# Optimization experiments

Hardware: AMD Instinct MI355X
Metric: run time of the kernel (lower is better)

## Reference

```python
import jax, jax.numpy as jnp
import numpy as np

N_NODES = 100000
N_EDGES = 1600000
D_IN, D_HID, D_OUT = 128, 128, 64


def spmm(row, col, val, h, n):
    # y[i] = sum_{e: row[e]==i} val[e] * h[col[e]]  (A_hat @ h with A in COO form)
    return jax.ops.segment_sum(val[:, None] * h[col], row, num_segments=n)


def setup_inputs() -> dict:
    key = jax.random.key(0)
    ks = jax.random.split(key, 7)
    x = jax.random.normal(ks[0], (1, N_NODES, D_IN), dtype=jnp.float32)
    edge_row = jax.random.randint(ks[1], (N_EDGES,), 0, N_NODES, dtype=jnp.int32)
    edge_col = jax.random.randint(ks[2], (N_EDGES,), 0, N_NODES, dtype=jnp.int32)
    edge_val = jax.random.uniform(ks[3], (N_EDGES,), dtype=jnp.float32)
    W0 = jax.random.normal(ks[4], (D_HID, D_IN), dtype=jnp.float32) * 0.05
    W1 = jax.random.normal(ks[5], (D_HID, D_HID), dtype=jnp.float32) * 0.05
    W2 = jax.random.normal(ks[6], (D_OUT, D_HID), dtype=jnp.float32) * 0.05
    return {"x": x, "edge_row": edge_row, "edge_col": edge_col,
            "edge_val": edge_val, "W0": W0, "W1": W1, "W2": W2}


def reference(x, edge_row, edge_col, edge_val, W0, W1, W2):
    B, N, D = x.shape
    n = B * N
    h = x.reshape(n, D)
    # input conv: Linear (no bias) -> SpMM -> ReLU
    h = jax.nn.relu(spmm(edge_row, edge_col, edge_val, h @ W0.T, n))
    # hidden conv with residual: ReLU(A (h W1^T)) + h
    h = jax.nn.relu(spmm(edge_row, edge_col, edge_val, h @ W1.T, n)) + h
    # dropout is identity in eval mode
    out = spmm(edge_row, edge_col, edge_val, h @ W2.T, n)
    return out
```

## Files before the change

kernel.cpp:

```cpp
#include <hip/hip_runtime.h>


typedef unsigned int u32;
typedef unsigned short u16;
typedef __attribute__((ext_vector_type(8))) short bf16x8;
typedef __attribute__((ext_vector_type(4))) float f32x4;

constexpr int NN = 100000;
constexpr int NE = 1600000;
constexpr int PAD = 100352;
constexpr int NBUCK = 196;
constexpr int BCAP = 10240;
constexpr int EPB = 2048;

__device__ __forceinline__ u16 f2bf(float f) {
    u32 x = __float_as_uint(f);
    x += 0x7fffu + ((x >> 16) & 1u);
    return (u16)(x >> 16);
}

template<int DO, bool FP32IN>
__global__ __launch_bounds__(256)
void gemm_mfma(const void* __restrict__ Hin, const u16* __restrict__ Wf,
               u16* __restrict__ Cb, int n)
{
    constexpr int RS   = 136;
    constexpr int PADW = DO + 8;
    __shared__ u16 smem[64 * 136];
    u16* sA = smem;
    u16* sC = smem;

    const int tid  = threadIdx.x;
    const int w    = tid >> 6;
    const int lane = tid & 63;
    const int m    = lane & 15;
    const int q    = lane >> 4;
    const int rowBase = blockIdx.x * 64;

    if (FP32IN) {
        const float* H = (const float*)Hin;
        #pragma unroll
        for (int i = 0; i < 8; ++i) {
            const int g = (i * 256 + tid) * 4;
            const int r = g >> 7, c = g & 127;
            float4 v = make_float4(0.f, 0.f, 0.f, 0.f);
            if (rowBase + r < n) v = *(const float4*)(H + (size_t)(rowBase + r) * 128 + c);
            u16* d = &sA[r * RS + c];
            d[0] = f2bf(v.x); d[1] = f2bf(v.y); d[2] = f2bf(v.z); d[3] = f2bf(v.w);
        }
    } else {
        const u16* H = (const u16*)Hin;
        #pragma unroll
        for (int i = 0; i < 4; ++i) {
            const int g = (i * 256 + tid) * 8;
            const int r = g >> 7, c = g & 127;
            uint4 v = make_uint4(0, 0, 0, 0);
            if (rowBase + r < n) v = *(const uint4*)(H + (size_t)(rowBase + r) * 128 + c);
            *(uint4*)&sA[r * RS + c] = v;
        }
    }
    __syncthreads();

    bf16x8 afrag[4];
    #pragma unroll
    for (int kc = 0; kc < 4; ++kc)
        afrag[kc] = *(const bf16x8*)&sA[(w * 16 + m) * RS + kc * 32 + q * 8];
    __syncthreads();

    #pragma unroll
    for (int ct = 0; ct < DO / 16; ++ct) {
        f32x4 acc = {0.f, 0.f, 0.f, 0.f};
        #pragma unroll
        for (int kc = 0; kc < 4; ++kc) {
            const bf16x8 b = *(const bf16x8*)(Wf + (((ct * 4 + kc) * 64) + lane) * 8);
            acc = __builtin_amdgcn_mfma_f32_16x16x32_bf16(afrag[kc], b, acc, 0, 0, 0);
        }
        #pragma unroll
        for (int r = 0; r < 4; ++r)
            sC[(w * 16 + q * 4 + r) * PADW + ct * 16 + m] = f2bf(acc[r]);
    }
    __syncthreads();

    const int g    = lane >> 2;
    const int cb   = (lane & 3) * (DO / 4);
    const int grow = rowBase + w * 16 + g;
    if (grow < n) {
        #pragma unroll
        for (int i = 0; i < DO / 32; ++i) {
            const int4 v = *(const int4*)&sC[(w * 16 + g) * PADW + cb + i * 8];
            *(int4*)(Cb + (size_t)grow * DO + cb + i * 8) = v;
        }
    }
}

__device__ __forceinline__ void wfrag_one(const float* __restrict__ W,
                                          u16* __restrict__ Wf, int total, int i)
{
    if (i < total) {
        const int j    = i & 7;
        const int lane = (i >> 3) & 63;
        const int kc   = (i >> 9) & 3;
        const int ct   = i >> 11;
        const int src  = (ct * 16 + (lane & 15)) * 128 + kc * 32 + (lane >> 4) * 8 + j;
        Wf[i] = f2bf(W[src]);
    }
}

__global__ __launch_bounds__(256)
void wcvt_kernel(const float* __restrict__ W0, const float* __restrict__ W1,
                 const float* __restrict__ W2, u16* __restrict__ wf0,
                 u16* __restrict__ wf1, u16* __restrict__ wf2)
{
    const int i = blockIdx.x * 256 + threadIdx.x;
    wfrag_one(W0, wf0, 128 * 128, i);
    wfrag_one(W1, wf1, 128 * 128, i);
    wfrag_one(W2, wf2, 64 * 128, i);
}

__global__ __launch_bounds__(256)
void part1_kernel(const int* __restrict__ erow, const int* __restrict__ ecol,
                  const float* __restrict__ eval, int* __restrict__ bcur,
                  int2* __restrict__ part)
{
    __shared__ int shist[NBUCK];
    __shared__ int sbase[NBUCK];
    const int tid = threadIdx.x;
    for (int i = tid; i < NBUCK; i += 256) shist[i] = 0;
    __syncthreads();

    const int base = blockIdx.x * EPB;
    #pragma unroll
    for (int j = 0; j < EPB / 256; ++j) {
        const int e = base + j * 256 + tid;
        if (e < NE) atomicAdd(&shist[erow[e] >> 9], 1);
    }
    __syncthreads();
    for (int i = tid; i < NBUCK; i += 256) {
        const int c = shist[i];
        sbase[i] = c ? atomicAdd(&bcur[i], c) : 0;
        shist[i] = 0;
    }
    __syncthreads();
    #pragma unroll
    for (int j = 0; j < EPB / 256; ++j) {
        const int e = base + j * 256 + tid;
        if (e < NE) {
            const int r = erow[e];
            const int b = r >> 9;
            const int rk = atomicAdd(&shist[b], 1);
            part[b * BCAP + sbase[b] + rk] =
                make_int2(((r & 511) << 17) | ecol[e], __float_as_int(eval[e]));
        }
    }
}

__global__ __launch_bounds__(256)
void part2_kernel(const int* __restrict__ bcur, const int2* __restrict__ part,
                  int* __restrict__ offs, int2* __restrict__ pce)
{
    __shared__ int scnt[512];
    __shared__ int sdata[256];
    __shared__ int rowoff[512];
    const int b = blockIdx.x;
    const int tid = threadIdx.x;

    const int bv = (tid < NBUCK) ? bcur[tid] : 0;
    sdata[tid] = bv;
    __syncthreads();
    #pragma unroll
    for (int off = 1; off < 256; off <<= 1) {
        const int val = (tid >= off) ? sdata[tid - off] : 0;
        __syncthreads();
        sdata[tid] += val;
        __syncthreads();
    }
    const int gb = (b > 0) ? sdata[b - 1] : 0;
    const int cnt = bcur[b];
    __syncthreads();

    scnt[tid] = 0; scnt[tid + 256] = 0;
    __syncthreads();

    const int2* src = part + (size_t)b * BCAP;
    for (int i = tid; i < cnt; i += 256)
        atomicAdd(&scnt[((u32)src[i].x) >> 17], 1);
    __syncthreads();

    const int c0 = scnt[2 * tid];
    const int c1 = scnt[2 * tid + 1];
    const int tsum = c0 + c1;
    sdata[tid] = tsum;
    __syncthreads();
    #pragma unroll
    for (int off = 1; off < 256; off <<= 1) {
        const int val = (tid >= off) ? sdata[tid - off] : 0;
        __syncthreads();
        sdata[tid] += val;
        __syncthreads();
    }
    const int excl = sdata[tid] - tsum;
    rowoff[2 * tid]     = gb + excl;
    rowoff[2 * tid + 1] = gb + excl + c0;
    __syncthreads();

    offs[b * 512 + tid]       = rowoff[tid];
    offs[b * 512 + 256 + tid] = rowoff[tid + 256];
    __syncthreads();

    for (int i = tid; i < cnt; i += 256) {
        const int2 ev = src[i];
        const int rl = ((u32)ev.x) >> 17;
        const int pos = atomicAdd(&rowoff[rl], 1);
        pce[pos] = make_int2(ev.x & 0x1FFFF, ev.y);
    }
}

template<int LPC>
__device__ __forceinline__ void load_row(const u16* p, u32* u) {
    if constexpr (LPC == 8) {
        const uint4 t = *(const uint4*)p;
        u[0] = t.x; u[1] = t.y; u[2] = t.z; u[3] = t.w;
    } else {
        const uint2 t = *(const uint2*)p;
        u[0] = t.x; u[1] = t.y;
    }
}

template<int LPC>
__device__ __forceinline__ void fma_row(float v, const u32* u, float* a) {
    #pragma unroll
    for (int j = 0; j < LPC / 2; ++j) {
        a[2*j]   = fmaf(v, __uint_as_float(u[j] << 16),         a[2*j]);
        a[2*j+1] = fmaf(v, __uint_as_float(u[j] & 0xffff0000u), a[2*j+1]);
    }
}

template<int DO, int MODE>
__global__ __launch_bounds__(256)
void spmm_gemm(const int* __restrict__ offs, const int2* __restrict__ pce,
               const u16* __restrict__ Hb, const u16* __restrict__ Wf,
               const u16* __restrict__ Res, u16* __restrict__ Cb,
               u16* __restrict__ Hout)
{
    constexpr int RS   = 136;
    constexpr int PADW = DO + 8;
    __shared__ u16 smem[16 * 136];
    const int tid = threadIdx.x;
    const int ln  = tid & 15;
    const int rl  = tid >> 4;
    const int row = blockIdx.x * 16 + rl;

    const int s = offs[row];
    const int t = offs[row + 1];
    const u16* hbase = Hb + ln * 8;

    float a0[8], a1[8];
    #pragma unroll
    for (int j = 0; j < 8; ++j) { a0[j] = 0.f; a1[j] = 0.f; }

    int e = s;
    for (; e + 1 < t; e += 2) {
        const int2 e0 = pce[e];
        const int2 e1 = pce[e + 1];
        u32 u0[4], u1[4];
        load_row<8>(hbase + (size_t)e0.x * 128, u0);
        load_row<8>(hbase + (size_t)e1.x * 128, u1);
        fma_row<8>(__int_as_float(e0.y), u0, a0);
        fma_row<8>(__int_as_float(e1.y), u1, a1);
    }
    if (e < t) {
        const int2 e0 = pce[e];
        u32 u0[4];
        load_row<8>(hbase + (size_t)e0.x * 128, u0);
        fma_row<8>(__int_as_float(e0.y), u0, a0);
    }
    #pragma unroll
    for (int j = 0; j < 8; ++j) a0[j] = fmaxf(a0[j] + a1[j], 0.f);

    if constexpr (MODE == 2) {
        u32 r[4];
        load_row<8>(Res + (size_t)row * 128 + ln * 8, r);
        #pragma unroll
        for (int j = 0; j < 4; ++j) {
            a0[2*j]   += __uint_as_float(r[j] << 16);
            a0[2*j+1] += __uint_as_float(r[j] & 0xffff0000u);
        }
    }
    u32 o[4];
    #pragma unroll
    for (int j = 0; j < 4; ++j)
        o[j] = (u32)f2bf(a0[2*j]) | ((u32)f2bf(a0[2*j+1]) << 16);
    const uint4 packed = make_uint4(o[0], o[1], o[2], o[3]);
    *(uint4*)&smem[rl * RS + ln * 8] = packed;
    if constexpr (MODE == 1)
        *(uint4*)(Hout + (size_t)row * 128 + ln * 8) = packed;
    __syncthreads();

    constexpr int TPW = DO / 64;
    const int w    = tid >> 6;
    const int lane = tid & 63;
    const int m    = lane & 15;
    const int q    = lane >> 4;

    bf16x8 afrag[4];
    #pragma unroll
    for (int kc = 0; kc < 4; ++kc)
        afrag[kc] = *(const bf16x8*)&smem[m * RS + kc * 32 + q * 8];

    f32x4 acc[TPW];
    #pragma unroll
    for (int tw = 0; tw < TPW; ++tw) {
        const int ct = w * TPW + tw;
        acc[tw] = (f32x4){0.f, 0.f, 0.f, 0.f};
        #pragma unroll
        for (int kc = 0; kc < 4; ++kc) {
            const bf16x8 b = *(const bf16x8*)(Wf + (((ct * 4 + kc) * 64) + lane) * 8);
            acc[tw] = __builtin_amdgcn_mfma_f32_16x16x32_bf16(afrag[kc], b, acc[tw], 0, 0, 0);
        }
    }
    __syncthreads();

    #pragma unroll
    for (int tw = 0; tw < TPW; ++tw) {
        const int ct = w * TPW + tw;
        #pragma unroll
        for (int r = 0; r < 4; ++r)
            smem[(q * 4 + r) * PADW + ct * 16 + m] = f2bf(acc[tw][r]);
    }
    __syncthreads();

    if (DO == 128 || tid < 128) {
        const int g = tid * 8;
        const int r = g / DO;
        const int c = g % DO;
        const int4 v = *(const int4*)&smem[r * PADW + c];
        *(int4*)(Cb + ((size_t)blockIdx.x * 16 + r) * DO + c) = v;
    }
}

__global__ __launch_bounds__(256)
void spmm_out(const int* __restrict__ offs, const int2* __restrict__ pce,
              const u16* __restrict__ Hb, float* __restrict__ Y)
{
    const int ln  = threadIdx.x & 15;
    const int row = blockIdx.x * 16 + (threadIdx.x >> 4);
    if (row >= NN) return;
    const int s = offs[row];
    const int t = offs[row + 1];
    const u16* hbase = Hb + ln * 4;

    float a0[4], a1[4];
    #pragma unroll
    for (int j = 0; j < 4; ++j) { a0[j] = 0.f; a1[j] = 0.f; }

    int e = s;
    for (; e + 1 < t; e += 2) {
        const int2 e0 = pce[e];
        const int2 e1 = pce[e + 1];
        u32 u0[2], u1[2];
        load_row<4>(hbase + (size_t)e0.x * 64, u0);
        load_row<4>(hbase + (size_t)e1.x * 64, u1);
        fma_row<4>(__int_as_float(e0.y), u0, a0);
        fma_row<4>(__int_as_float(e1.y), u1, a1);
    }
    if (e < t) {
        const int2 e0 = pce[e];
        u32 u0[2];
        load_row<4>(hbase + (size_t)e0.x * 64, u0);
        fma_row<4>(__int_as_float(e0.y), u0, a0);
    }
    #pragma unroll
    for (int j = 0; j < 4; ++j) a0[j] += a1[j];
    *(float4*)(Y + (size_t)row * 64 + ln * 4) = make_float4(a0[0], a0[1], a0[2], a0[3]);
}

extern "C" void kernel_launch(void* const* d_in, const int* in_sizes, int n_in,
                              void* d_out, int out_size, void* d_ws, size_t ws_size,
                              hipStream_t stream) {
    const float* x    = (const float*)d_in[0];
    const int*   erow = (const int*)  d_in[1];
    const int*   ecol = (const int*)  d_in[2];
    const float* eval = (const float*)d_in[3];
    const float* W0   = (const float*)d_in[4];
    const float* W1   = (const float*)d_in[5];
    const float* W2   = (const float*)d_in[6];
    float* out = (float*)d_out;

    char* p = (char*)d_ws;
    const size_t BUFB = (size_t)NN * 128 * sizeof(u16);
    u16* t0b  = (u16*)p;  p += BUFB;
    u16* t1b  = (u16*)p;  p += BUFB;
    u16* h1b  = (u16*)p;  p += BUFB;
    u16* wf0  = (u16*)p;  p += 128 * 128 * 2;
    u16* wf1  = (u16*)p;  p += 128 * 128 * 2;
    u16* wf2  = (u16*)p;  p += 64 * 128 * 2;
    int* bcur   = (int*)p; p += 256 * 4;
    int* offs   = (int*)p; p += ((size_t)PAD + 256) * 4;
    int2* part  = (int2*)p; p += (size_t)NBUCK * BCAP * 8;
    int2* pce   = (int2*)p;

    const dim3 blk(256);
    const int gemmBlocks  = (NN + 63) / 64;
    const int rowBlocks   = NN / 16;
    const int part1Blocks = (NE + EPB - 1) / EPB;

    hipMemsetAsync(bcur, 0, 256 * 4, stream);
    part1_kernel<<<part1Blocks, blk, 0, stream>>>(erow, ecol, eval, bcur, part);
    part2_kernel<<<NBUCK, blk, 0, stream>>>(bcur, part, offs, pce);
    wcvt_kernel <<<64, blk, 0, stream>>>(W0, W1, W2, wf0, wf1, wf2);

    gemm_mfma<128, true><<<gemmBlocks, blk, 0, stream>>>(x, wf0, t0b, NN);
    spmm_gemm<128, 1><<<rowBlocks, blk, 0, stream>>>(offs, pce, t0b, wf1, nullptr, t1b, h1b);
    spmm_gemm<64, 2><<<rowBlocks, blk, 0, stream>>>(offs, pce, t1b, wf2, h1b, t0b, nullptr);
    spmm_out<<<rowBlocks, blk, 0, stream>>>(offs, pce, t0b, out);
}
```

Before: 364.6 us.

## Merge edge partition pass and first GEMM into one kernel launch

Folds the first edge-bucketing pass and the first-layer x@W0 GEMM into a single kernel whose block range is split between the two jobs, so independent work runs concurrently. The memset of the bucket counters moves into the weight-conversion kernel, which now runs first, removing a launch. EPB is doubled, halving the partition blocks and the global atomics on the bucket counters, at the cost of more serial work per block. The aim is fewer launches and better GPU fill; the fused kernel's shared memory is sized for the GEMM path, which may limit occupancy for the partition blocks.

```diff
diff --git a/kernel.cpp b/kernel.cpp
--- a/kernel.cpp
+++ b/kernel.cpp
@@ -11,86 +11,14 @@
 constexpr int PAD = 100352;
 constexpr int NBUCK = 196;
 constexpr int BCAP = 10240;
-constexpr int EPB = 2048;
+constexpr int EPB = 4096;
+constexpr int P1B = (NE + EPB - 1) / EPB;
+constexpr int G0B = (NN + 63) / 64;
 
 __device__ __forceinline__ u16 f2bf(float f) {
     u32 x = __float_as_uint(f);
     x += 0x7fffu + ((x >> 16) & 1u);
     return (u16)(x >> 16);
-}
-
-template<int DO, bool FP32IN>
-__global__ __launch_bounds__(256)
-void gemm_mfma(const void* __restrict__ Hin, const u16* __restrict__ Wf,
-               u16* __restrict__ Cb, int n)
-{
-    constexpr int RS   = 136;
-    constexpr int PADW = DO + 8;
-    __shared__ u16 smem[64 * 136];
-    u16* sA = smem;
-    u16* sC = smem;
-
-    const int tid  = threadIdx.x;
-    const int w    = tid >> 6;
-    const int lane = tid & 63;
-    const int m    = lane & 15;
-    const int q    = lane >> 4;
-    const int rowBase = blockIdx.x * 64;
-
-    if (FP32IN) {
-        const float* H = (const float*)Hin;
-        #pragma unroll
-        for (int i = 0; i < 8; ++i) {
-            const int g = (i * 256 + tid) * 4;
-            const int r = g >> 7, c = g & 127;
-            float4 v = make_float4(0.f, 0.f, 0.f, 0.f);
-            if (rowBase + r < n) v = *(const float4*)(H + (size_t)(rowBase + r) * 128 + c);
-            u16* d = &sA[r * RS + c];
-            d[0] = f2bf(v.x); d[1] = f2bf(v.y); d[2] = f2bf(v.z); d[3] = f2bf(v.w);
-        }
-    } else {
-        const u16* H = (const u16*)Hin;
-        #pragma unroll
-        for (int i = 0; i < 4; ++i) {
-            const int g = (i * 256 + tid) * 8;
-            const int r = g >> 7, c = g & 127;
-            uint4 v = make_uint4(0, 0, 0, 0);
-            if (rowBase + r < n) v = *(const uint4*)(H + (size_t)(rowBase + r) * 128 + c);
-            *(uint4*)&sA[r * RS + c] = v;
-        }
-    }
-    __syncthreads();
-
-    bf16x8 afrag[4];
-    #pragma unroll
-    for (int kc = 0; kc < 4; ++kc)
-        afrag[kc] = *(const bf16x8*)&sA[(w * 16 + m) * RS + kc * 32 + q * 8];
-    __syncthreads();
-
-    #pragma unroll
-    for (int ct = 0; ct < DO / 16; ++ct) {
-        f32x4 acc = {0.f, 0.f, 0.f, 0.f};
-        #pragma unroll
-        for (int kc = 0; kc < 4; ++kc) {
-            const bf16x8 b = *(const bf16x8*)(Wf + (((ct * 4 + kc) * 64) + lane) * 8);
-            acc = __builtin_amdgcn_mfma_f32_16x16x32_bf16(afrag[kc], b, acc, 0, 0, 0);
-        }
-        #pragma unroll
-        for (int r = 0; r < 4; ++r)
-            sC[(w * 16 + q * 4 + r) * PADW + ct * 16 + m] = f2bf(acc[r]);
-    }
-    __syncthreads();
-
-    const int g    = lane >> 2;
-    const int cb   = (lane & 3) * (DO / 4);
-    const int grow = rowBase + w * 16 + g;
-    if (grow < n) {
-        #pragma unroll
-        for (int i = 0; i < DO / 32; ++i) {
-            const int4 v = *(const int4*)&sC[(w * 16 + g) * PADW + cb + i * 8];
-            *(int4*)(Cb + (size_t)grow * DO + cb + i * 8) = v;
-        }
-    }
 }
 
 __device__ __forceinline__ void wfrag_one(const float* __restrict__ W,
@@ -109,47 +37,108 @@
 __global__ __launch_bounds__(256)
 void wcvt_kernel(const float* __restrict__ W0, const float* __restrict__ W1,
                  const float* __restrict__ W2, u16* __restrict__ wf0,
-                 u16* __restrict__ wf1, u16* __restrict__ wf2)
+                 u16* __restrict__ wf1, u16* __restrict__ wf2,
+                 int* __restrict__ bcur)
 {
     const int i = blockIdx.x * 256 + threadIdx.x;
+    if (blockIdx.x == 0) bcur[threadIdx.x] = 0;
     wfrag_one(W0, wf0, 128 * 128, i);
     wfrag_one(W1, wf1, 128 * 128, i);
     wfrag_one(W2, wf2, 64 * 128, i);
 }
 
 __global__ __launch_bounds__(256)
-void part1_kernel(const int* __restrict__ erow, const int* __restrict__ ecol,
-                  const float* __restrict__ eval, int* __restrict__ bcur,
-                  int2* __restrict__ part)
-{
-    __shared__ int shist[NBUCK];
-    __shared__ int sbase[NBUCK];
+void k1_kernel(const float* __restrict__ x, const u16* __restrict__ Wf,
+               u16* __restrict__ Cb,
+               const int* __restrict__ erow, const int* __restrict__ ecol,
+               const float* __restrict__ eval, int* __restrict__ bcur,
+               int2* __restrict__ part)
+{
+    __shared__ u16 smem[64 * 136];
     const int tid = threadIdx.x;
-    for (int i = tid; i < NBUCK; i += 256) shist[i] = 0;
-    __syncthreads();
-
-    const int base = blockIdx.x * EPB;
-    #pragma unroll
-    for (int j = 0; j < EPB / 256; ++j) {
-        const int e = base + j * 256 + tid;
-        if (e < NE) atomicAdd(&shist[erow[e] >> 9], 1);
-    }
-    __syncthreads();
-    for (int i = tid; i < NBUCK; i += 256) {
-        const int c = shist[i];
-        sbase[i] = c ? atomicAdd(&bcur[i], c) : 0;
-        shist[i] = 0;
-    }
-    __syncthreads();
-    #pragma unroll
-    for (int j = 0; j < EPB / 256; ++j) {
-        const int e = base + j * 256 + tid;
-        if (e < NE) {
-            const int r = erow[e];
-            const int b = r >> 9;
-            const int rk = atomicAdd(&shist[b], 1);
-            part[b * BCAP + sbase[b] + rk] =
-                make_int2(((r & 511) << 17) | ecol[e], __float_as_int(eval[e]));
+
+    if ((int)blockIdx.x < P1B) {
+        int* shist = (int*)smem;
+        int* sbase = shist + NBUCK;
+        for (int i = tid; i < NBUCK; i += 256) shist[i] = 0;
+        __syncthreads();
+
+        const int base = blockIdx.x * EPB;
+        #pragma unroll
+        for (int j = 0; j < EPB / 256; ++j) {
+            const int e = base + j * 256 + tid;
+            if (e < NE) atomicAdd(&shist[erow[e] >> 9], 1);
+        }
+        __syncthreads();
+        for (int i = tid; i < NBUCK; i += 256) {
+            const int c = shist[i];
+            sbase[i] = c ? atomicAdd(&bcur[i], c) : 0;
+            shist[i] = 0;
+        }
+        __syncthreads();
+        #pragma unroll
+        for (int j = 0; j < EPB / 256; ++j) {
+            const int e = base + j * 256 + tid;
+            if (e < NE) {
+                const int r = erow[e];
+                const int b = r >> 9;
+                const int rk = atomicAdd(&shist[b], 1);
+                part[b * BCAP + sbase[b] + rk] =
+                    make_int2(((r & 511) << 17) | ecol[e], __float_as_int(eval[e]));
+            }
+        }
+        return;
+    }
+
+    constexpr int RS   = 136;
+    constexpr int PADW = 136;
+    u16* sA = smem;
+    u16* sC = smem;
+    const int w    = tid >> 6;
+    const int lane = tid & 63;
+    const int m    = lane & 15;
+    const int q    = lane >> 4;
+    const int rowBase = ((int)blockIdx.x - P1B) * 64;
+
+    #pragma unroll
+    for (int i = 0; i < 8; ++i) {
+        const int g = (i * 256 + tid) * 4;
+        const int r = g >> 7, c = g & 127;
+        float4 v = make_float4(0.f, 0.f, 0.f, 0.f);
+        if (rowBase + r < NN) v = *(const float4*)(x + (size_t)(rowBase + r) * 128 + c);
+        u16* d = &sA[r * RS + c];
+        d[0] = f2bf(v.x); d[1] = f2bf(v.y); d[2] = f2bf(v.z); d[3] = f2bf(v.w);
+    }
+    __syncthreads();
+
+    bf16x8 afrag[4];
+    #pragma unroll
+    for (int kc = 0; kc < 4; ++kc)
+        afrag[kc] = *(const bf16x8*)&sA[(w * 16 + m) * RS + kc * 32 + q * 8];
+    __syncthreads();
+
+    #pragma unroll
+    for (int ct = 0; ct < 8; ++ct) {
+        f32x4 acc = {0.f, 0.f, 0.f, 0.f};
+        #pragma unroll
+        for (int kc = 0; kc < 4; ++kc) {
+            const bf16x8 b = *(const bf16x8*)(Wf + (((ct * 4 + kc) * 64) + lane) * 8);
+            acc = __builtin_amdgcn_mfma_f32_16x16x32_bf16(afrag[kc], b, acc, 0, 0, 0);
+        }
+        #pragma unroll
+        for (int r = 0; r < 4; ++r)
+            sC[(w * 16 + q * 4 + r) * PADW + ct * 16 + m] = f2bf(acc[r]);
+    }
+    __syncthreads();
+
+    const int g    = lane >> 2;
+    const int cb   = (lane & 3) * 32;
+    const int grow = rowBase + w * 16 + g;
+    if (grow < NN) {
+        #pragma unroll
+        for (int i = 0; i < 4; ++i) {
+            const int4 v = *(const int4*)&sC[(w * 16 + g) * PADW + cb + i * 8];
+            *(int4*)(Cb + (size_t)grow * 128 + cb + i * 8) = v;
         }
     }
 }
@@ -400,16 +389,11 @@
     int2* pce   = (int2*)p;
 
     const dim3 blk(256);
-    const int gemmBlocks  = (NN + 63) / 64;
-    const int rowBlocks   = NN / 16;
-    const int part1Blocks = (NE + EPB - 1) / EPB;
-
-    hipMemsetAsync(bcur, 0, 256 * 4, stream);
-    part1_kernel<<<part1Blocks, blk, 0, stream>>>(erow, ecol, eval, bcur, part);
+    const int rowBlocks = NN / 16;
+
+    wcvt_kernel<<<64, blk, 0, stream>>>(W0, W1, W2, wf0, wf1, wf2, bcur);
+    k1_kernel  <<<P1B + G0B, blk, 0, stream>>>(x, wf0, t0b, erow, ecol, eval, bcur, part);
     part2_kernel<<<NBUCK, blk, 0, stream>>>(bcur, part, offs, pce);
-    wcvt_kernel <<<64, blk, 0, stream>>>(W0, W1, W2, wf0, wf1, wf2);
-
-    gemm_mfma<128, true><<<gemmBlocks, blk, 0, stream>>>(x, wf0, t0b, NN);
     spmm_gemm<128, 1><<<rowBlocks, blk, 0, stream>>>(offs, pce, t0b, wf1, nullptr, t1b, h1b);
     spmm_gemm<64, 2><<<rowBlocks, blk, 0, stream>>>(offs, pce, t1b, wf2, h1b, t0b, nullptr);
     spmm_out<<<rowBlocks, blk, 0, stream>>>(offs, pce, t0b, out);
```

After: 356.5 us. 2.2% less time.
